# Kernel tuning notes

Measured on AMD Instinct MI355X. Metric: run time of the kernel, lower is better.

## Reference

```python
import jax, jax.numpy as jnp
import numpy as np

B, T, N_MODEL, HEAD_SIZE = 8, 4096, 1024, 128


def setup_inputs() -> dict:
    key = jax.random.key(0)
    k1, k2 = jax.random.split(key)
    x = jax.random.normal(k1, (B, T, N_MODEL), dtype=jnp.float32)
    W_K = jax.random.normal(k2, (HEAD_SIZE, N_MODEL), dtype=jnp.float32) * 0.02
    return {"x": x, "W_K": W_K}


def _rope_inplace_semantics(t, cos, sin):
    """Replicates the source's in-place slice writes:
    even' = t1*cos + t2*sin  (written first)
    odd'  = -even'*sin + t2*cos  (t1 view already holds even' when read)
    """
    t1 = t[..., ::2]
    t2 = t[..., 1::2]
    even = t1 * cos + t2 * sin
    odd = -even * sin + t2 * cos
    # re-interleave: [..., half, 2] -> [..., head_size]
    return jnp.stack([even, odd], axis=-1).reshape(t.shape)


def reference(x, W_K):
    head_size = W_K.shape[0]
    T_len = x.shape[-2]
    half = head_size // 2
    # frequency-only thetas (no position index, as in source)
    thetas = jnp.power(10000.0, -(jnp.arange(half, dtype=jnp.float32) / half))
    cos = jnp.cos(thetas)
    sin = jnp.sin(thetas)

    # NOTE: source uses self.K for k, q AND v (faithful to the bug)
    k = x @ W_K.T  # [B, T, head_size]
    v = k
    k_rot = _rope_inplace_semantics(k, cos, sin)
    q_rot = k_rot  # q computed identically from K(x)

    # w[i,j] = k_i . q_j (k first, as in source einsum)
    w = jnp.einsum('bik,bjk->bij', k_rot, q_rot) * (head_size ** -0.5)
    mask = jnp.triu(jnp.full((T_len, T_len), -jnp.inf, dtype=w.dtype), k=1)
    w = jax.nn.softmax(w + mask, axis=-1)
    out = jnp.einsum('bij,bjk->bik', w, v)  # [B, T, head_size]
    return out
```

## Files before the change

kernel.cpp:

```cpp
#include <hip/hip_runtime.h>
#include <hip/hip_bf16.h>
#include <cstdint>
#include <cmath>

typedef __attribute__((ext_vector_type(8))) __bf16 bf16x8;
typedef __attribute__((ext_vector_type(8))) _Float16 f16x8;
typedef __attribute__((ext_vector_type(4))) float f32x4;
typedef __attribute__((ext_vector_type(16))) float f32x16;
typedef __attribute__((ext_vector_type(4))) int i32x4;
typedef __attribute__((ext_vector_type(16))) int i32x16;

typedef const __attribute__((address_space(1))) void* as1cvp;
typedef __attribute__((address_space(3))) void* as3vp;

__device__ __forceinline__ void gload_lds16(const void* g, void* l) {
  __builtin_amdgcn_global_load_lds((as1cvp)g, (as3vp)l, 16, 0, 0);
}
__device__ __forceinline__ float readlane_f(float v, int l) {
  return __uint_as_float((uint32_t)__builtin_amdgcn_readlane((int)__float_as_uint(v), l));
}

#define QS     (3.9f / 127.0f)
#define INVQS  (127.0f / 3.9f)
#define C1     (QS * QS * 0.12751706f)
#define SMBIAS 12.0f

__device__ __forceinline__ f16x8 dq8(uint64_t v) {
  union { uint32_t u[4]; f16x8 h; } r;
  uint32_t lo = (uint32_t)v, hi = (uint32_t)(v >> 32);
  r.u[0] = __builtin_amdgcn_perm(0x64646464u, lo, 0x04010400u);
  r.u[1] = __builtin_amdgcn_perm(0x64646464u, lo, 0x04030402u);
  r.u[2] = __builtin_amdgcn_perm(0x64646464u, hi, 0x04010400u);
  r.u[3] = __builtin_amdgcn_perm(0x64646464u, hi, 0x04030402u);
  return r.h;
}

__device__ __forceinline__ int vperm(int p) {
  return 16 * (p >> 4) + 4 * ((p >> 3) & 1) + 8 * ((p >> 2) & 1) + (p & 3);
}

__global__ __launch_bounds__(256) void wk_convert_kernel(
    const float* __restrict__ wk, __bf16* __restrict__ wkbf) {
  int i = (blockIdx.x * 256 + threadIdx.x) * 4;
  f32x4 v = *(const f32x4*)(wk + i);
  union { __bf16 e[4]; uint64_t u; } p;
#pragma unroll
  for (int j = 0; j < 4; j++) p.e[j] = (__bf16)v[j];
  *(uint64_t*)(wkbf + i) = p.u;
}

__global__ __launch_bounds__(256, 4) void proj_rope_kernel(
    const float* __restrict__ x, const __bf16* __restrict__ wkbf,
    char* __restrict__ k2i8, unsigned char* __restrict__ vt3u8)
{
  __shared__ __align__(16) char psmem[40960];
  const int tid = threadIdx.x;
  const int wid = tid >> 6;
  const int lane = tid & 63;
  const int m0 = blockIdx.x * 32;
  const int wn = wid * 32;

  f32x4 acc[2][2];
#pragma unroll
  for (int i = 0; i < 2; i++)
#pragma unroll
    for (int j = 0; j < 2; j++) acc[i][j] = (f32x4)0.f;

  const int ar = tid >> 3, ac = (tid & 7) * 8;
  const float* gx0 = x + (size_t)(m0 + ar) * 1024 + ac;

  f32x4 pa0, pa1;
#define LOADA(K0) do { const float* gp = gx0 + (K0); pa0 = *(const f32x4*)gp; pa1 = *(const f32x4*)(gp + 4); } while (0)
#define WRITEA(BUF) do { \
    bf16x8 av; \
    _Pragma("unroll") for (int jj = 0; jj < 4; jj++) { av[jj] = (__bf16)pa0[jj]; av[4 + jj] = (__bf16)pa1[jj]; } \
    *(bf16x8*)((__bf16*)psmem + (BUF) * 2048 + ar * 64 + (ac ^ ((ar & 7) << 3))) = av; \
  } while (0)
#define STAGEB(BUF, K0) do { \
    _Pragma("unroll") for (int h = 0; h < 4; h++) { \
      int Lc = tid + h * 256; int row = Lc >> 3, sp = Lc & 7; \
      gload_lds16((const char*)wkbf + row * 2048 + (K0) * 2 + ((sp ^ (row & 7)) << 4), \
                  psmem + 8192 + (BUF) * 16384 + Lc * 16); \
    } } while (0)

  LOADA(0);
  STAGEB(0, 0);
  WRITEA(0);
  __syncthreads();

  for (int t = 0; t < 16; t++) {
    const int buf = t & 1;
    const bool more = (t + 1 < 16);
    if (more) { LOADA((t + 1) * 64); STAGEB(buf ^ 1, (t + 1) * 64); }
    const __bf16* As = (const __bf16*)psmem + buf * 2048;
    const __bf16* Bs = (const __bf16*)(psmem + 8192 + buf * 16384);
#pragma unroll
    for (int kk = 0; kk < 2; kk++) {
      bf16x8 afr[2], bfr[2];
#pragma unroll
      for (int mi = 0; mi < 2; mi++) {
        int row = mi * 16 + (lane & 15);
        int col = (kk * 32 + (lane >> 4) * 8) ^ ((row & 7) << 3);
        afr[mi] = *(const bf16x8*)&As[row * 64 + col];
      }
#pragma unroll
      for (int ni = 0; ni < 2; ni++) {
        int row = wn + ni * 16 + (lane & 15);
        int col = (kk * 32 + (lane >> 4) * 8) ^ ((row & 7) << 3);
        bfr[ni] = *(const bf16x8*)&Bs[row * 64 + col];
      }
#pragma unroll
      for (int mi = 0; mi < 2; mi++)
#pragma unroll
        for (int ni = 0; ni < 2; ni++)
          acc[mi][ni] = __builtin_amdgcn_mfma_f32_16x16x32_bf16(afr[mi], bfr[ni], acc[mi][ni], 0, 0, 0);
    }
    if (more) WRITEA(buf ^ 1);
    __syncthreads();
  }

  float cosv[2], sinv[2];
#pragma unroll
  for (int ni = 0; ni < 2; ni++) {
    int d = wn + ni * 16 + (lane & 15);
    float theta = exp2f((float)(d >> 1) * -0.20762050593046014f);
    cosv[ni] = cosf(theta);
    sinv[ni] = sinf(theta);
  }
  unsigned char* vl8 = (unsigned char*)psmem;
  char* kl8 = psmem + 8192;
  const bool evenlane = ((lane & 1) == 0);
#pragma unroll
  for (int mi = 0; mi < 2; mi++) {
#pragma unroll
    for (int r = 0; r < 4; r++) {
      int ml = mi * 16 + (lane >> 4) * 4 + r;
#pragma unroll
      for (int ni = 0; ni < 2; ni++) {
        float val = acc[mi][ni][r];
        int d = wn + ni * 16 + (lane & 15);
        int uv = (int)lrintf(fminf(fmaxf(val * INVQS, -127.f), 127.f)) + 128;
        vl8[ml * 128 + d] = (unsigned char)uv;
        float partner = __shfl_xor(val, 1);
        float e = evenlane ? val : partner;
        float o = evenlane ? partner : val;
        float ev = e * cosv[ni] + o * sinv[ni];
        float od = -ev * sinv[ni] + o * cosv[ni];
        float kr = evenlane ? ev : od;
        int qv = (int)lrintf(fminf(fmaxf(kr * INVQS, -127.f), 127.f));
        kl8[ml * 128 + (((d >> 4) ^ (ml & 7)) << 4) + (d & 15)] = (char)qv;
      }
    }
  }
  __syncthreads();
  const size_t T = blockIdx.x;
  {
    int s = tid >> 5, kv = tid & 31;
    i32x4 w = *(const i32x4*)(kl8 + kv * 128 + ((s ^ (kv & 7)) << 4));
    *(i32x4*)(k2i8 + T * 4096 + s * 512 + kv * 16) = w;
  }
  {
    int d = tid >> 1, th = tid & 1;
    unsigned char* vg = vt3u8 + T * 4096 + d * 8;
#pragma unroll
    for (int cc = 0; cc < 2; cc++) {
      int c = 2 * th + cc;
      union { unsigned char b[8]; uint64_t u; } w;
#pragma unroll
      for (int jj = 0; jj < 8; jj++)
        w.b[jj] = vl8[vperm(c * 8 + jj) * 128 + d];
      *(uint64_t*)(vg + c * 1024) = w.u;
    }
  }
}

__global__ __launch_bounds__(256) void attn_kernel(
    const char* __restrict__ k2i8, const unsigned char* __restrict__ vt3u8,
    float* __restrict__ out)
{
  __shared__ __align__(16) char smem[33152];
  const int tid = threadIdx.x;
  const int split = tid >> 6;
  const int lane = tid & 63;
  const int lo5 = lane & 31;
  const int hi = lane >> 5;
  const int b = blockIdx.x & 7;
  const int g = (int)(blockIdx.x >> 3);
  const char* kt8 = k2i8 + (size_t)b * 524288;
  const unsigned char* vb8 = vt3u8 + (size_t)b * 524288;
  float* ob = out + (size_t)b * 4096 * 128;

  float* mA = (float*)smem;
  float* mB = (float*)(smem + 16384);
  float* lbuf = (float*)(smem + 32768);

#pragma unroll 1
  for (int pass = 0; pass < 2; pass++) {
    const int qt = pass ? (127 - g) : g;
    const int q0 = qt * 32;
    const int jd = qt;

    i32x4 qf8[4];
    {
      const char* qp = kt8 + (size_t)qt * 4096 + lo5 * 16;
#pragma unroll
      for (int ks = 0; ks < 4; ks++) qf8[ks] = *(const i32x4*)(qp + (2 * ks + hi) * 512);
    }

    f32x16 acc[4];
#pragma unroll
    for (int dt = 0; dt < 4; dt++) acc[dt] = (f32x16)0.f;
    float l_r = 0.f;

    for (int j = split; j <= jd; j += 4) {
      const char* kp8 = kt8 + (size_t)j * 4096 + lo5 * 16;
      const unsigned char* vp8 = vb8 + (size_t)j * 4096 + lo5 * 8;
      i32x4 kf8[4];
#pragma unroll
      for (int ks = 0; ks < 4; ks++) kf8[ks] = *(const i32x4*)(kp8 + (2 * ks + hi) * 512);
      uint64_t vu0[4], vu1[4];
#pragma unroll
      for (int dt = 0; dt < 4; dt++) {
        vu0[dt] = *(const uint64_t*)(vp8 + hi * 1024 + dt * 256);
        vu1[dt] = *(const uint64_t*)(vp8 + (2 + hi) * 1024 + dt * 256);
      }
      i32x16 S0i = (i32x16)0, S1i = (i32x16)0;
      __builtin_amdgcn_s_setprio(1);
      S0i = __builtin_amdgcn_mfma_i32_32x32x32_i8(kf8[0], qf8[0], S0i, 0, 0, 0);
      S0i = __builtin_amdgcn_mfma_i32_32x32x32_i8(kf8[1], qf8[1], S0i, 0, 0, 0);
      S1i = __builtin_amdgcn_mfma_i32_32x32x32_i8(kf8[2], qf8[2], S1i, 0, 0, 0);
      S1i = __builtin_amdgcn_mfma_i32_32x32x32_i8(kf8[3], qf8[3], S1i, 0, 0, 0);
      __builtin_amdgcn_s_setprio(0);
      f32x16 S;
#pragma unroll
      for (int r = 0; r < 16; r++)
        S[r] = fmaf((float)(S0i[r] + S1i[r]), C1, -SMBIAS);
      if (j == jd) {
        const int kv0 = j * 32;
#pragma unroll
        for (int r = 0; r < 16; r++) {
          int kvg = kv0 + (r & 3) + 8 * (r >> 2) + 4 * hi;
          if (kvg > q0 + lo5) S[r] = -1e30f;
        }
      }
      union U { _Float16 e[8]; f16x8 v; };
      U pk0, pk1;
      float rs = 0.f;
#pragma unroll
      for (int jj = 0; jj < 8; jj++) { float p = exp2f(S[jj]); rs += p; pk0.e[jj] = (_Float16)p; }
#pragma unroll
      for (int jj = 0; jj < 8; jj++) { float p = exp2f(S[8 + jj]); rs += p; pk1.e[jj] = (_Float16)p; }
      l_r += rs;
      __builtin_amdgcn_s_setprio(1);
#pragma unroll
      for (int dt = 0; dt < 4; dt++)
        acc[dt] = __builtin_amdgcn_mfma_f32_32x32x16_f16(pk0.v, dq8(vu0[dt]), acc[dt], 0, 0, 0);
#pragma unroll
      for (int dt = 0; dt < 4; dt++)
        acc[dt] = __builtin_amdgcn_mfma_f32_32x32x16_f16(pk1.v, dq8(vu1[dt]), acc[dt], 0, 0, 0);
      __builtin_amdgcn_s_setprio(0);
    }
    l_r += __shfl_xor(l_r, 32);

#define ACC_TO(M) do { \
      _Pragma("unroll") for (int r = 0; r < 16; r++) { \
        int ql_ = (r & 3) + 8 * (r >> 2) + 4 * hi; \
        _Pragma("unroll") for (int dt = 0; dt < 4; dt++) (M)[ql_ * 128 + dt * 32 + lo5] = acc[dt][r]; } \
    } while (0)
#define ACC_ADD(M) do { \
      _Pragma("unroll") for (int r = 0; r < 16; r++) { \
        int ql_ = (r & 3) + 8 * (r >> 2) + 4 * hi; \
        _Pragma("unroll") for (int dt = 0; dt < 4; dt++) acc[dt][r] += (M)[ql_ * 128 + dt * 32 + lo5]; } \
    } while (0)
    if (split == 1) { ACC_TO(mA); if (lane < 32) lbuf[lane] = l_r; }
    if (split == 3) { ACC_TO(mB); if (lane < 32) lbuf[64 + lane] = l_r; }
    __syncthreads();
    if (split == 0) { ACC_ADD(mA); l_r += lbuf[lo5]; }
    if (split == 2) { ACC_ADD(mB); l_r += lbuf[64 + lo5]; }
    __syncthreads();
    if (split == 2) { ACC_TO(mA); if (lane < 32) lbuf[32 + lane] = l_r; }
    __syncthreads();
    if (split == 0) {
      ACC_ADD(mA);
      l_r += lbuf[32 + lo5];
      float invl = 1.0f / l_r;
#pragma unroll
      for (int r = 0; r < 16; r++) {
        const int rb = (r & 3) + 8 * (r >> 2);
        float ivr = hi ? readlane_f(invl, rb + 4) : readlane_f(invl, rb);
        const int ql = rb + 4 * hi;
        const size_t qg = (size_t)(q0 + ql);
#pragma unroll
        for (int dt = 0; dt < 4; dt++)
          ob[qg * 128 + dt * 32 + lo5] = (acc[dt][r] * ivr - 1152.0f) * QS;
      }
    }
    __syncthreads();
  }
}

extern "C" void kernel_launch(void* const* d_in, const int* in_sizes, int n_in,
                              void* d_out, int out_size, void* d_ws, size_t ws_size,
                              hipStream_t stream) {
  const float* x  = (const float*)d_in[0];
  const float* wk = (const float*)d_in[1];
  char* k2i8 = (char*)d_ws;
  unsigned char* vt3u8 = (unsigned char*)d_ws + (size_t)4 * 1024 * 1024;
  float* out   = (float*)d_out;
  __bf16* wkbf = (__bf16*)d_out;
  wk_convert_kernel<<<128, 256, 0, stream>>>(wk, wkbf);
  proj_rope_kernel<<<1024, 256, 0, stream>>>(x, wkbf, k2i8, vt3u8);
  attn_kernel<<<512, 256, 0, stream>>>(k2i8, vt3u8, out);
}
```

Before: 85.68 us.

## Repack V tiles for 16-byte loads and double-buffer attention tile loads

The projection kernel now writes each V tile so that a lane's two 8-byte V fragments sit next to each other. The attention kernel can then fetch them with one 16-byte load per dt instead of two 8-byte loads. The attention loop is unrolled by two with separate register sets, so the K and V loads for two tiles are issued before either is computed, which gives more memory-level parallelism to hide global load latency. The cost is higher register pressure from the doubled fragment buffers, which could lower occupancy.

New measurement: 107.7 us. 25.7% more time.

```diff
diff --git a/kernel.cpp b/kernel.cpp
--- a/kernel.cpp
+++ b/kernel.cpp
@@ -9,6 +9,7 @@
 typedef __attribute__((ext_vector_type(16))) float f32x16;
 typedef __attribute__((ext_vector_type(4))) int i32x4;
 typedef __attribute__((ext_vector_type(16))) int i32x16;
+typedef __attribute__((ext_vector_type(2))) unsigned long long u64x2;
 
 typedef const __attribute__((address_space(1))) void* as1cvp;
 typedef __attribute__((address_space(3))) void* as3vp;
@@ -51,7 +52,7 @@
 
 __global__ __launch_bounds__(256, 4) void proj_rope_kernel(
     const float* __restrict__ x, const __bf16* __restrict__ wkbf,
-    char* __restrict__ k2i8, unsigned char* __restrict__ vt3u8)
+    char* __restrict__ k2i8, unsigned char* __restrict__ vt4u8)
 {
   __shared__ __align__(16) char psmem[40960];
   const int tid = threadIdx.x;
@@ -161,21 +162,18 @@
   }
   {
     int d = tid >> 1, th = tid & 1;
-    unsigned char* vg = vt3u8 + T * 4096 + d * 8;
-#pragma unroll
-    for (int cc = 0; cc < 2; cc++) {
-      int c = 2 * th + cc;
-      union { unsigned char b[8]; uint64_t u; } w;
-#pragma unroll
-      for (int jj = 0; jj < 8; jj++)
-        w.b[jj] = vl8[vperm(c * 8 + jj) * 128 + d];
-      *(uint64_t*)(vg + c * 1024) = w.u;
-    }
+    union { unsigned char b[16]; i32x4 q; } w;
+#pragma unroll
+    for (int jj = 0; jj < 8; jj++) {
+      w.b[jj]     = vl8[vperm(th * 8 + jj) * 128 + d];
+      w.b[8 + jj] = vl8[vperm((th + 2) * 8 + jj) * 128 + d];
+    }
+    *(i32x4*)(vt4u8 + T * 4096 + th * 2048 + d * 16) = w.q;
   }
 }
 
 __global__ __launch_bounds__(256) void attn_kernel(
-    const char* __restrict__ k2i8, const unsigned char* __restrict__ vt3u8,
+    const char* __restrict__ k2i8, const unsigned char* __restrict__ vt4u8,
     float* __restrict__ out)
 {
   __shared__ __align__(16) char smem[33152];
@@ -187,7 +185,7 @@
   const int b = blockIdx.x & 7;
   const int g = (int)(blockIdx.x >> 3);
   const char* kt8 = k2i8 + (size_t)b * 524288;
-  const unsigned char* vb8 = vt3u8 + (size_t)b * 524288;
+  const unsigned char* vb8 = vt4u8 + (size_t)b * 524288;
   float* ob = out + (size_t)b * 4096 * 128;
 
   float* mA = (float*)smem;
@@ -212,53 +210,57 @@
     for (int dt = 0; dt < 4; dt++) acc[dt] = (f32x16)0.f;
     float l_r = 0.f;
 
-    for (int j = split; j <= jd; j += 4) {
-      const char* kp8 = kt8 + (size_t)j * 4096 + lo5 * 16;
-      const unsigned char* vp8 = vb8 + (size_t)j * 4096 + lo5 * 8;
-      i32x4 kf8[4];
-#pragma unroll
-      for (int ks = 0; ks < 4; ks++) kf8[ks] = *(const i32x4*)(kp8 + (2 * ks + hi) * 512);
-      uint64_t vu0[4], vu1[4];
-#pragma unroll
-      for (int dt = 0; dt < 4; dt++) {
-        vu0[dt] = *(const uint64_t*)(vp8 + hi * 1024 + dt * 256);
-        vu1[dt] = *(const uint64_t*)(vp8 + (2 + hi) * 1024 + dt * 256);
-      }
-      i32x16 S0i = (i32x16)0, S1i = (i32x16)0;
-      __builtin_amdgcn_s_setprio(1);
-      S0i = __builtin_amdgcn_mfma_i32_32x32x32_i8(kf8[0], qf8[0], S0i, 0, 0, 0);
-      S0i = __builtin_amdgcn_mfma_i32_32x32x32_i8(kf8[1], qf8[1], S0i, 0, 0, 0);
-      S1i = __builtin_amdgcn_mfma_i32_32x32x32_i8(kf8[2], qf8[2], S1i, 0, 0, 0);
-      S1i = __builtin_amdgcn_mfma_i32_32x32x32_i8(kf8[3], qf8[3], S1i, 0, 0, 0);
-      __builtin_amdgcn_s_setprio(0);
-      f32x16 S;
-#pragma unroll
-      for (int r = 0; r < 16; r++)
-        S[r] = fmaf((float)(S0i[r] + S1i[r]), C1, -SMBIAS);
-      if (j == jd) {
-        const int kv0 = j * 32;
-#pragma unroll
-        for (int r = 0; r < 16; r++) {
-          int kvg = kv0 + (r & 3) + 8 * (r >> 2) + 4 * hi;
-          if (kvg > q0 + lo5) S[r] = -1e30f;
-        }
-      }
-      union U { _Float16 e[8]; f16x8 v; };
-      U pk0, pk1;
-      float rs = 0.f;
-#pragma unroll
-      for (int jj = 0; jj < 8; jj++) { float p = exp2f(S[jj]); rs += p; pk0.e[jj] = (_Float16)p; }
-#pragma unroll
-      for (int jj = 0; jj < 8; jj++) { float p = exp2f(S[8 + jj]); rs += p; pk1.e[jj] = (_Float16)p; }
-      l_r += rs;
-      __builtin_amdgcn_s_setprio(1);
-#pragma unroll
-      for (int dt = 0; dt < 4; dt++)
-        acc[dt] = __builtin_amdgcn_mfma_f32_32x32x16_f16(pk0.v, dq8(vu0[dt]), acc[dt], 0, 0, 0);
-#pragma unroll
-      for (int dt = 0; dt < 4; dt++)
-        acc[dt] = __builtin_amdgcn_mfma_f32_32x32x16_f16(pk1.v, dq8(vu1[dt]), acc[dt], 0, 0, 0);
-      __builtin_amdgcn_s_setprio(0);
+#define LOADT(KF, VU, J) do { \
+      const char* kp_ = kt8 + (size_t)(J) * 4096 + lo5 * 16; \
+      const unsigned char* vp_ = vb8 + (size_t)(J) * 4096 + hi * 2048 + lo5 * 16; \
+      _Pragma("unroll") for (int ks = 0; ks < 4; ks++) KF[ks] = *(const i32x4*)(kp_ + (2 * ks + hi) * 512); \
+      _Pragma("unroll") for (int dt = 0; dt < 4; dt++) VU[dt] = *(const u64x2*)(vp_ + dt * 512); \
+    } while (0)
+
+#define COMPT(KF, VU, J) do { \
+      i32x16 S0i_ = (i32x16)0, S1i_ = (i32x16)0; \
+      __builtin_amdgcn_s_setprio(1); \
+      S0i_ = __builtin_amdgcn_mfma_i32_32x32x32_i8(KF[0], qf8[0], S0i_, 0, 0, 0); \
+      S0i_ = __builtin_amdgcn_mfma_i32_32x32x32_i8(KF[1], qf8[1], S0i_, 0, 0, 0); \
+      S1i_ = __builtin_amdgcn_mfma_i32_32x32x32_i8(KF[2], qf8[2], S1i_, 0, 0, 0); \
+      S1i_ = __builtin_amdgcn_mfma_i32_32x32x32_i8(KF[3], qf8[3], S1i_, 0, 0, 0); \
+      __builtin_amdgcn_s_setprio(0); \
+      f32x16 S_; \
+      _Pragma("unroll") for (int r = 0; r < 16; r++) \
+        S_[r] = fmaf((float)(S0i_[r] + S1i_[r]), C1, -SMBIAS); \
+      if ((J) == jd) { \
+        const int kv0_ = (J) * 32; \
+        _Pragma("unroll") for (int r = 0; r < 16; r++) { \
+          int kvg_ = kv0_ + (r & 3) + 8 * (r >> 2) + 4 * hi; \
+          if (kvg_ > q0 + lo5) S_[r] = -1e30f; \
+        } \
+      } \
+      union Upk_ { _Float16 e[8]; f16x8 v; }; \
+      Upk_ pk0_, pk1_; \
+      float rs_ = 0.f; \
+      _Pragma("unroll") for (int jj = 0; jj < 8; jj++) { float p_ = exp2f(S_[jj]); rs_ += p_; pk0_.e[jj] = (_Float16)p_; } \
+      _Pragma("unroll") for (int jj = 0; jj < 8; jj++) { float p_ = exp2f(S_[8 + jj]); rs_ += p_; pk1_.e[jj] = (_Float16)p_; } \
+      l_r += rs_; \
+      __builtin_amdgcn_s_setprio(1); \
+      _Pragma("unroll") for (int dt = 0; dt < 4; dt++) \
+        acc[dt] = __builtin_amdgcn_mfma_f32_32x32x16_f16(pk0_.v, dq8(VU[dt].x), acc[dt], 0, 0, 0); \
+      _Pragma("unroll") for (int dt = 0; dt < 4; dt++) \
+        acc[dt] = __builtin_amdgcn_mfma_f32_32x32x16_f16(pk1_.v, dq8(VU[dt].y), acc[dt], 0, 0, 0); \
+      __builtin_amdgcn_s_setprio(0); \
+    } while (0)
+
+    i32x4 kfA[4], kfB[4];
+    u64x2 vuA[4], vuB[4];
+    int j = split;
+    for (; j + 4 <= jd; j += 8) {
+      LOADT(kfA, vuA, j);
+      LOADT(kfB, vuB, j + 4);
+      COMPT(kfA, vuA, j);
+      COMPT(kfB, vuB, j + 4);
+    }
+    if (j <= jd) {
+      LOADT(kfA, vuA, j);
+      COMPT(kfA, vuA, j);
     }
     l_r += __shfl_xor(l_r, 32);
 
@@ -305,10 +307,10 @@
   const float* x  = (const float*)d_in[0];
   const float* wk = (const float*)d_in[1];
   char* k2i8 = (char*)d_ws;
-  unsigned char* vt3u8 = (unsigned char*)d_ws + (size_t)4 * 1024 * 1024;
+  unsigned char* vt4u8 = (unsigned char*)d_ws + (size_t)4 * 1024 * 1024;
   float* out   = (float*)d_out;
   __bf16* wkbf = (__bf16*)d_out;
   wk_convert_kernel<<<128, 256, 0, stream>>>(wk, wkbf);
-  proj_rope_kernel<<<1024, 256, 0, stream>>>(x, wkbf, k2i8, vt3u8);
-  attn_kernel<<<512, 256, 0, stream>>>(k2i8, vt3u8, out);
-}
+  proj_rope_kernel<<<1024, 256, 0, stream>>>(x, wkbf, k2i8, vt4u8);
+  attn_kernel<<<512, 256, 0, stream>>>(k2i8, vt4u8, out);
+}
```

## Split attention blocks into two 3-wave query-tile groups with repacked V layout

Applied to the files above, without the earlier changes.

The attention kernel now runs 384 threads per block as two sub-groups of three waves, each handling its own query tile, so a block covers two query tiles per pass and the KV loop is split three ways instead of four. The V tensor is repacked so each lane fetches one 16-byte vector per dt instead of two 8-byte loads. The two int8 QK accumulators are merged into a single chained MFMA accumulator, and the cross-wave reduction drops from three barriers to one. Shared memory doubles to about 66KB per block, which may limit occupancy. Longer serial KV chains per wave could reduce latency hiding.

New measurement: 148.8 us. 1.74x slower.

```diff
diff --git a/kernel.cpp b/kernel.cpp
--- a/kernel.cpp
+++ b/kernel.cpp
@@ -9,6 +9,7 @@
 typedef __attribute__((ext_vector_type(16))) float f32x16;
 typedef __attribute__((ext_vector_type(4))) int i32x4;
 typedef __attribute__((ext_vector_type(16))) int i32x16;
+typedef __attribute__((ext_vector_type(2))) unsigned long long u64x2;
 
 typedef const __attribute__((address_space(1))) void* as1cvp;
 typedef __attribute__((address_space(3))) void* as3vp;
@@ -51,7 +52,7 @@
 
 __global__ __launch_bounds__(256, 4) void proj_rope_kernel(
     const float* __restrict__ x, const __bf16* __restrict__ wkbf,
-    char* __restrict__ k2i8, unsigned char* __restrict__ vt3u8)
+    char* __restrict__ k2i8, unsigned char* __restrict__ vt4u8)
 {
   __shared__ __align__(16) char psmem[40960];
   const int tid = threadIdx.x;
@@ -161,42 +162,41 @@
   }
   {
     int d = tid >> 1, th = tid & 1;
-    unsigned char* vg = vt3u8 + T * 4096 + d * 8;
-#pragma unroll
-    for (int cc = 0; cc < 2; cc++) {
-      int c = 2 * th + cc;
-      union { unsigned char b[8]; uint64_t u; } w;
-#pragma unroll
-      for (int jj = 0; jj < 8; jj++)
-        w.b[jj] = vl8[vperm(c * 8 + jj) * 128 + d];
-      *(uint64_t*)(vg + c * 1024) = w.u;
-    }
-  }
-}
-
-__global__ __launch_bounds__(256) void attn_kernel(
-    const char* __restrict__ k2i8, const unsigned char* __restrict__ vt3u8,
+    union { unsigned char b[16]; i32x4 q; } w;
+#pragma unroll
+    for (int jj = 0; jj < 8; jj++) {
+      w.b[jj]     = vl8[vperm(th * 8 + jj) * 128 + d];
+      w.b[8 + jj] = vl8[vperm((th + 2) * 8 + jj) * 128 + d];
+    }
+    *(i32x4*)(vt4u8 + T * 4096 + th * 2048 + d * 16) = w.q;
+  }
+}
+
+__global__ __launch_bounds__(384, 3) void attn_kernel(
+    const char* __restrict__ k2i8, const unsigned char* __restrict__ vt4u8,
     float* __restrict__ out)
 {
-  __shared__ __align__(16) char smem[33152];
+  __shared__ __align__(16) char smem[66048];
   const int tid = threadIdx.x;
-  const int split = tid >> 6;
+  const int wid = tid >> 6;
+  const int sub = (wid >= 3) ? 1 : 0;
+  const int sp = wid - 3 * sub;
   const int lane = tid & 63;
   const int lo5 = lane & 31;
   const int hi = lane >> 5;
   const int b = blockIdx.x & 7;
-  const int g = (int)(blockIdx.x >> 3);
+  const int G = (int)(blockIdx.x >> 3);
   const char* kt8 = k2i8 + (size_t)b * 524288;
-  const unsigned char* vb8 = vt3u8 + (size_t)b * 524288;
+  const unsigned char* vb8 = vt4u8 + (size_t)b * 524288;
   float* ob = out + (size_t)b * 4096 * 128;
 
-  float* mA = (float*)smem;
-  float* mB = (float*)(smem + 16384);
-  float* lbuf = (float*)(smem + 32768);
+  float* m0s = (float*)(smem + sub * 32768);
+  float* m1s = (float*)(smem + sub * 32768 + 16384);
+  float* lbuf = (float*)(smem + 65536) + sub * 64;
 
 #pragma unroll 1
   for (int pass = 0; pass < 2; pass++) {
-    const int qt = pass ? (127 - g) : g;
+    const int qt = pass ? (126 - 2 * G + sub) : (2 * G + sub);
     const int q0 = qt * 32;
     const int jd = qt;
 
@@ -212,29 +212,26 @@
     for (int dt = 0; dt < 4; dt++) acc[dt] = (f32x16)0.f;
     float l_r = 0.f;
 
-    for (int j = split; j <= jd; j += 4) {
+    for (int j = sp; j <= jd; j += 3) {
       const char* kp8 = kt8 + (size_t)j * 4096 + lo5 * 16;
-      const unsigned char* vp8 = vb8 + (size_t)j * 4096 + lo5 * 8;
+      const unsigned char* vp8 = vb8 + (size_t)j * 4096 + hi * 2048 + lo5 * 16;
       i32x4 kf8[4];
 #pragma unroll
       for (int ks = 0; ks < 4; ks++) kf8[ks] = *(const i32x4*)(kp8 + (2 * ks + hi) * 512);
-      uint64_t vu0[4], vu1[4];
-#pragma unroll
-      for (int dt = 0; dt < 4; dt++) {
-        vu0[dt] = *(const uint64_t*)(vp8 + hi * 1024 + dt * 256);
-        vu1[dt] = *(const uint64_t*)(vp8 + (2 + hi) * 1024 + dt * 256);
-      }
-      i32x16 S0i = (i32x16)0, S1i = (i32x16)0;
+      u64x2 vu[4];
+#pragma unroll
+      for (int dt = 0; dt < 4; dt++) vu[dt] = *(const u64x2*)(vp8 + dt * 512);
+      i32x16 Si = (i32x16)0;
       __builtin_amdgcn_s_setprio(1);
-      S0i = __builtin_amdgcn_mfma_i32_32x32x32_i8(kf8[0], qf8[0], S0i, 0, 0, 0);
-      S0i = __builtin_amdgcn_mfma_i32_32x32x32_i8(kf8[1], qf8[1], S0i, 0, 0, 0);
-      S1i = __builtin_amdgcn_mfma_i32_32x32x32_i8(kf8[2], qf8[2], S1i, 0, 0, 0);
-      S1i = __builtin_amdgcn_mfma_i32_32x32x32_i8(kf8[3], qf8[3], S1i, 0, 0, 0);
+      Si = __builtin_amdgcn_mfma_i32_32x32x32_i8(kf8[0], qf8[0], Si, 0, 0, 0);
+      Si = __builtin_amdgcn_mfma_i32_32x32x32_i8(kf8[1], qf8[1], Si, 0, 0, 0);
+      Si = __builtin_amdgcn_mfma_i32_32x32x32_i8(kf8[2], qf8[2], Si, 0, 0, 0);
+      Si = __builtin_amdgcn_mfma_i32_32x32x32_i8(kf8[3], qf8[3], Si, 0, 0, 0);
       __builtin_amdgcn_s_setprio(0);
       f32x16 S;
 #pragma unroll
       for (int r = 0; r < 16; r++)
-        S[r] = fmaf((float)(S0i[r] + S1i[r]), C1, -SMBIAS);
+        S[r] = fmaf((float)Si[r], C1, -SMBIAS);
       if (j == jd) {
         const int kv0 = j * 32;
 #pragma unroll
@@ -254,10 +251,10 @@
       __builtin_amdgcn_s_setprio(1);
 #pragma unroll
       for (int dt = 0; dt < 4; dt++)
-        acc[dt] = __builtin_amdgcn_mfma_f32_32x32x16_f16(pk0.v, dq8(vu0[dt]), acc[dt], 0, 0, 0);
+        acc[dt] = __builtin_amdgcn_mfma_f32_32x32x16_f16(pk0.v, dq8(vu[dt].x), acc[dt], 0, 0, 0);
 #pragma unroll
       for (int dt = 0; dt < 4; dt++)
-        acc[dt] = __builtin_amdgcn_mfma_f32_32x32x16_f16(pk1.v, dq8(vu1[dt]), acc[dt], 0, 0, 0);
+        acc[dt] = __builtin_amdgcn_mfma_f32_32x32x16_f16(pk1.v, dq8(vu[dt].y), acc[dt], 0, 0, 0);
       __builtin_amdgcn_s_setprio(0);
     }
     l_r += __shfl_xor(l_r, 32);
@@ -267,22 +264,18 @@
         int ql_ = (r & 3) + 8 * (r >> 2) + 4 * hi; \
         _Pragma("unroll") for (int dt = 0; dt < 4; dt++) (M)[ql_ * 128 + dt * 32 + lo5] = acc[dt][r]; } \
     } while (0)
-#define ACC_ADD(M) do { \
+#define ACC_ADD2(MA, MB) do { \
       _Pragma("unroll") for (int r = 0; r < 16; r++) { \
         int ql_ = (r & 3) + 8 * (r >> 2) + 4 * hi; \
-        _Pragma("unroll") for (int dt = 0; dt < 4; dt++) acc[dt][r] += (M)[ql_ * 128 + dt * 32 + lo5]; } \
+        _Pragma("unroll") for (int dt = 0; dt < 4; dt++) \
+          acc[dt][r] += (MA)[ql_ * 128 + dt * 32 + lo5] + (MB)[ql_ * 128 + dt * 32 + lo5]; } \
     } while (0)
-    if (split == 1) { ACC_TO(mA); if (lane < 32) lbuf[lane] = l_r; }
-    if (split == 3) { ACC_TO(mB); if (lane < 32) lbuf[64 + lane] = l_r; }
+    if (sp == 1) { ACC_TO(m0s); if (lane < 32) lbuf[lane] = l_r; }
+    if (sp == 2) { ACC_TO(m1s); if (lane < 32) lbuf[32 + lane] = l_r; }
     __syncthreads();
-    if (split == 0) { ACC_ADD(mA); l_r += lbuf[lo5]; }
-    if (split == 2) { ACC_ADD(mB); l_r += lbuf[64 + lo5]; }
-    __syncthreads();
-    if (split == 2) { ACC_TO(mA); if (lane < 32) lbuf[32 + lane] = l_r; }
-    __syncthreads();
-    if (split == 0) {
-      ACC_ADD(mA);
-      l_r += lbuf[32 + lo5];
+    if (sp == 0) {
+      ACC_ADD2(m0s, m1s);
+      l_r += lbuf[lo5] + lbuf[32 + lo5];
       float invl = 1.0f / l_r;
 #pragma unroll
       for (int r = 0; r < 16; r++) {
@@ -305,10 +298,10 @@
   const float* x  = (const float*)d_in[0];
   const float* wk = (const float*)d_in[1];
   char* k2i8 = (char*)d_ws;
-  unsigned char* vt3u8 = (unsigned char*)d_ws + (size_t)4 * 1024 * 1024;
+  unsigned char* vt4u8 = (unsigned char*)d_ws + (size_t)4 * 1024 * 1024;
   float* out   = (float*)d_out;
   __bf16* wkbf = (__bf16*)d_out;
   wk_convert_kernel<<<128, 256, 0, stream>>>(wk, wkbf);
-  proj_rope_kernel<<<1024, 256, 0, stream>>>(x, wkbf, k2i8, vt3u8);
-  attn_kernel<<<512, 256, 0, stream>>>(k2i8, vt3u8, out);
-}
+  proj_rope_kernel<<<1024, 256, 0, stream>>>(x, wkbf, k2i8, vt4u8);
+  attn_kernel<<<512, 384, 0, stream>>>(k2i8, vt4u8, out);
+}
```
